# Performance work log

Measured on AMD Instinct MI355X. Metric: run time of the kernel, lower is better.

Reference implementation:

```python
import jax, jax.numpy as jnp
import numpy as np

N = 50000
E = 800000
D_IN, D_HID, D_OUT = 128, 128, 256


def _sage_layer(x, src, dst, W_l, b_l, W_r):
    # PyG SAGEConv: out = lin_l(mean_j x_j) + lin_r(x_i)
    msg = x[src]                                              # [E, d]
    agg = jax.ops.segment_sum(msg, dst, num_segments=x.shape[0])
    cnt = jax.ops.segment_sum(jnp.ones((src.shape[0],), x.dtype), dst,
                              num_segments=x.shape[0])
    mean = agg / jnp.maximum(cnt, 1.0)[:, None]
    return mean @ W_l.T + b_l + x @ W_r.T


def setup_inputs() -> dict:
    key = jax.random.key(0)
    ks = jax.random.split(key, 12)
    x = jax.random.normal(ks[0], (N, D_IN), dtype=jnp.float32)
    edge_index = jax.random.randint(ks[1], (2, E), 0, N, dtype=jnp.int64)

    def lin(k, out_d, in_d):
        s = 1.0 / np.sqrt(in_d)
        return jax.random.uniform(k, (out_d, in_d), jnp.float32, -s, s)

    return {
        "x": x,
        "edge_index": edge_index,
        "W_l0": lin(ks[2], D_HID, D_IN),
        "b_l0": jnp.zeros((D_HID,), jnp.float32),
        "W_r0": lin(ks[3], D_HID, D_IN),
        "W_l1": lin(ks[4], D_HID, D_HID),
        "b_l1": jnp.zeros((D_HID,), jnp.float32),
        "W_r1": lin(ks[5], D_HID, D_HID),
        "W_l2": lin(ks[6], D_OUT, D_HID),
        "b_l2": jnp.zeros((D_OUT,), jnp.float32),
        "W_r2": lin(ks[7], D_OUT, D_HID),
    }


def reference(x, edge_index, W_l0, b_l0, W_r0, W_l1, b_l1, W_r1, W_l2, b_l2, W_r2):
    src, dst = edge_index[0], edge_index[1]
    h = jax.nn.relu(_sage_layer(x, src, dst, W_l0, b_l0, W_r0))   # dropout = identity (eval)
    h = jax.nn.relu(_sage_layer(h, src, dst, W_l1, b_l1, W_r1))
    out = _sage_layer(h, src, dst, W_l2, b_l2, W_r2)
    return out
```

## Files before the change

kernel.cpp:

```cpp
#include <hip/hip_runtime.h>
#include <stdint.h>

typedef unsigned short u16;
typedef unsigned int   u32;
typedef __attribute__((ext_vector_type(8))) short short8;
typedef __attribute__((ext_vector_type(4))) float f32x4;

#define CHUNK 8192

__device__ __forceinline__ u16 f2bf(float f) {
    u32 u = __float_as_uint(f);
    u32 r = (u + 0x7FFFu + ((u >> 16) & 1u)) >> 16;
    return (u16)r;
}

__global__ void detect_fmt(const int* __restrict__ ei, int* __restrict__ flag,
                           int* __restrict__ offs, int N, int E) {
    if (blockIdx.x == 0 && threadIdx.x == 0) {
        int z = ei[1] | ei[3] | ei[5] | ei[7] | ei[9] | ei[11];
        flag[0] = (z == 0) ? 1 : 0;
        offs[N] = E;
    }
}

__global__ void zero_out(float* __restrict__ p, size_t n) {
    size_t i = (size_t)blockIdx.x * 256 + threadIdx.x;
    size_t stride = (size_t)gridDim.x * 256;
    for (; i < n; i += stride) p[i] = 0.f;
}

__global__ void hist_bucket(const int* __restrict__ ei, const int* __restrict__ flag,
                            int* __restrict__ cnt, int E, int N, int nb, int NBK) {
    __shared__ int h[256];
    int b = blockIdx.x, t = threadIdx.x;
    h[t] = 0;
    __syncthreads();
    int is64 = flag[0];
    int base = b * CHUNK;
    int endE = min(base + CHUNK, E);
    for (int i = base + t; i < endE; i += 256) {
        int dst = is64 ? ei[2 * E + 2 * i] : ei[E + i];
        dst = min(max(dst, 0), N - 1);
        atomicAdd(&h[dst >> 8], 1);
    }
    __syncthreads();
    for (int B = t; B < NBK; B += 256) cnt[B * nb + b] = h[B];
}

__global__ void scan_partial(const int* __restrict__ a, int* __restrict__ bsum, int M) {
    __shared__ int sh[256];
    int t = threadIdx.x;
    int idx0 = blockIdx.x * 1024 + t * 4;
    int s = 0;
    #pragma unroll
    for (int i = 0; i < 4; ++i) { int idx = idx0 + i; if (idx < M) s += a[idx]; }
    sh[t] = s;
    __syncthreads();
    #pragma unroll
    for (int off = 128; off > 0; off >>= 1) {
        if (t < off) sh[t] += sh[t + off];
        __syncthreads();
    }
    if (t == 0) bsum[blockIdx.x] = sh[0];
}

__global__ void scan_bsum(int* __restrict__ bsum, int nbs) {
    __shared__ int sh[256];
    __shared__ int carry;
    int t = threadIdx.x;
    if (t == 0) carry = 0;
    __syncthreads();
    for (int base = 0; base < nbs; base += 256) {
        int v = (base + t < nbs) ? bsum[base + t] : 0;
        sh[t] = v;
        __syncthreads();
        #pragma unroll
        for (int off = 1; off < 256; off <<= 1) {
            int x = (t >= off) ? sh[t - off] : 0;
            __syncthreads();
            sh[t] += x;
            __syncthreads();
        }
        if (base + t < nbs) bsum[base + t] = carry + sh[t] - v;
        __syncthreads();
        if (t == 255) carry += sh[255];
        __syncthreads();
    }
}

__global__ void scan_final(int* __restrict__ a, const int* __restrict__ bsum, int M) {
    __shared__ int sh[256];
    int t = threadIdx.x;
    int idx0 = blockIdx.x * 1024 + t * 4;
    int v[4];
    int s = 0;
    #pragma unroll
    for (int i = 0; i < 4; ++i) {
        int idx = idx0 + i;
        v[i] = (idx < M) ? a[idx] : 0;
        s += v[i];
    }
    sh[t] = s;
    __syncthreads();
    #pragma unroll
    for (int off = 1; off < 256; off <<= 1) {
        int x = (t >= off) ? sh[t - off] : 0;
        __syncthreads();
        sh[t] += x;
        __syncthreads();
    }
    int run = sh[t] - s + bsum[blockIdx.x];
    #pragma unroll
    for (int i = 0; i < 4; ++i) {
        int idx = idx0 + i;
        if (idx < M) a[idx] = run;
        run += v[i];
    }
}

__global__ void scatter_pairs(const int* __restrict__ ei, const int* __restrict__ flag,
                              const int* __restrict__ pboff, int2* __restrict__ pairs,
                              int E, int N, int nb, int NBK) {
    __shared__ int cur[256];
    int b = blockIdx.x, t = threadIdx.x;
    for (int B = t; B < NBK; B += 256) cur[B] = pboff[B * nb + b];
    __syncthreads();
    int is64 = flag[0];
    int base = b * CHUNK;
    int endE = min(base + CHUNK, E);
    for (int i = base + t; i < endE; i += 256) {
        int src = is64 ? ei[2 * i] : ei[i];
        int dst = is64 ? ei[2 * E + 2 * i] : ei[E + i];
        src = min(max(src, 0), N - 1);
        dst = min(max(dst, 0), N - 1);
        int slot = atomicAdd(&cur[dst >> 8], 1);
        pairs[slot] = make_int2(src, dst);
    }
}

__global__ void fine_sort(const int2* __restrict__ pairs, const int* __restrict__ pboff,
                          int* __restrict__ offs, int* __restrict__ ssrc,
                          int E, int N, int nb, int NBK) {
    __shared__ int hist[256];
    __shared__ int excl[256];
    __shared__ int cur[256];
    int B = blockIdx.x, t = threadIdx.x;
    int rs = pboff[B * nb];
    int re = (B + 1 < NBK) ? pboff[(B + 1) * nb] : E;
    hist[t] = 0;
    __syncthreads();
    for (int i = rs + t; i < re; i += 256) {
        int2 p = pairs[i];
        atomicAdd(&hist[p.y & 255], 1);
    }
    __syncthreads();
    int v = hist[t];
    excl[t] = v;
    __syncthreads();
    #pragma unroll
    for (int off = 1; off < 256; off <<= 1) {
        int x = (t >= off) ? excl[t - off] : 0;
        __syncthreads();
        excl[t] += x;
        __syncthreads();
    }
    int ex = excl[t] - v;
    int node = B * 256 + t;
    if (node < N) offs[node] = rs + ex;
    cur[t] = rs + ex;
    __syncthreads();
    for (int i = rs + t; i < re; i += 256) {
        int2 p = pairs[i];
        int slot = atomicAdd(&cur[p.y & 255], 1);
        ssrc[slot] = p.x;
    }
}

__global__ void conv_bf16(const float4* __restrict__ x, uint2* __restrict__ H, int n4) {
    int i = blockIdx.x * 256 + threadIdx.x;
    if (i >= n4) return;
    float4 v = x[i];
    uint2 o;
    o.x = ((u32)f2bf(v.y) << 16) | f2bf(v.x);
    o.y = ((u32)f2bf(v.w) << 16) | f2bf(v.z);
    H[i] = o;
}

__global__ void prep_w(const float* __restrict__ Wl, const float* __restrict__ Wr,
                       u16* __restrict__ Wc, int dout) {
    int i = blockIdx.x * 256 + threadIdx.x;
    if (i >= dout * 256) return;
    int j = i >> 8, k = i & 255;
    float v = (k < 128) ? Wl[j * 128 + k] : Wr[j * 128 + (k - 128)];
    Wc[i] = f2bf(v);
}

__device__ __forceinline__ void acc8(float* a, uint4 p) {
    a[0] += __uint_as_float(p.x << 16); a[1] += __uint_as_float(p.x & 0xFFFF0000u);
    a[2] += __uint_as_float(p.y << 16); a[3] += __uint_as_float(p.y & 0xFFFF0000u);
    a[4] += __uint_as_float(p.z << 16); a[5] += __uint_as_float(p.z & 0xFFFF0000u);
    a[6] += __uint_as_float(p.w << 16); a[7] += __uint_as_float(p.w & 0xFFFF0000u);
}

__global__ void aggregate(const u16* __restrict__ H, const int* __restrict__ offs,
                          const int* __restrict__ ssrc, u16* __restrict__ M, int N) {
    int node = blockIdx.x * 16 + (threadIdx.x >> 4);
    int sub  = threadIdx.x & 15;
    if (node >= N) return;
    int beg = offs[node], end = offs[node + 1];
    float a0[8] = {}, a1[8] = {}, a2[8] = {}, a3[8] = {};
    int j = beg;
    for (; j + 3 < end; j += 4) {
        int s0 = ssrc[j], s1 = ssrc[j + 1], s2 = ssrc[j + 2], s3 = ssrc[j + 3];
        uint4 p0 = *(const uint4*)(H + (size_t)s0 * 128 + sub * 8);
        uint4 p1 = *(const uint4*)(H + (size_t)s1 * 128 + sub * 8);
        uint4 p2 = *(const uint4*)(H + (size_t)s2 * 128 + sub * 8);
        uint4 p3 = *(const uint4*)(H + (size_t)s3 * 128 + sub * 8);
        acc8(a0, p0); acc8(a1, p1); acc8(a2, p2); acc8(a3, p3);
    }
    for (; j < end; ++j) {
        uint4 p0 = *(const uint4*)(H + (size_t)ssrc[j] * 128 + sub * 8);
        acc8(a0, p0);
    }
    int d = end - beg;
    float sc = 1.f / (float)(d > 0 ? d : 1);
    #pragma unroll
    for (int i = 0; i < 8; ++i) a0[i] = (a0[i] + a1[i] + a2[i] + a3[i]) * sc;
    uint4 o;
    o.x = ((u32)f2bf(a0[1]) << 16) | f2bf(a0[0]);
    o.y = ((u32)f2bf(a0[3]) << 16) | f2bf(a0[2]);
    o.z = ((u32)f2bf(a0[5]) << 16) | f2bf(a0[4]);
    o.w = ((u32)f2bf(a0[7]) << 16) | f2bf(a0[6]);
    *(uint4*)(M + (size_t)node * 128 + sub * 8) = o;
}

template<int DOUT, bool RELU, bool OUT_F32>
__global__ void gemm_mfma(const u16* __restrict__ M, const u16* __restrict__ H,
                          const u16* __restrict__ Wc, const float* __restrict__ bias,
                          void* __restrict__ out, int N) {
    int tid  = threadIdx.x;
    int w    = tid >> 6;
    int l    = tid & 63;
    int m_base = blockIdx.x * 128 + w * 32;
    int n_base = blockIdx.y * 128;

    int lr = l & 15;
    int lq = l >> 4;
    int kof = lq * 8;

    f32x4 acc[2][8];
    #pragma unroll
    for (int i = 0; i < 2; ++i)
        #pragma unroll
        for (int j = 0; j < 8; ++j) acc[i][j] = (f32x4){0.f, 0.f, 0.f, 0.f};

    int r0 = m_base + lr, r1 = r0 + 16;
    const short8 zf = (short8){0,0,0,0,0,0,0,0};

    #pragma unroll
    for (int ks = 0; ks < 8; ++ks) {
        const u16* Asrc = (ks < 4) ? M : H;
        int ka = (ks & 3) * 32 + kof;
        short8 a0 = (r0 < N) ? *(const short8*)(Asrc + (size_t)r0 * 128 + ka) : zf;
        short8 a1 = (r1 < N) ? *(const short8*)(Asrc + (size_t)r1 * 128 + ka) : zf;
        int kb = ks * 32 + kof;
        #pragma unroll
        for (int ct = 0; ct < 8; ++ct) {
            int wrow = n_base + ct * 16 + lr;
            short8 b = *(const short8*)(Wc + (size_t)wrow * 256 + kb);
            acc[0][ct] = __builtin_amdgcn_mfma_f32_16x16x32_bf16(a0, b, acc[0][ct], 0, 0, 0);
            acc[1][ct] = __builtin_amdgcn_mfma_f32_16x16x32_bf16(a1, b, acc[1][ct], 0, 0, 0);
        }
    }

    #pragma unroll
    for (int rg = 0; rg < 2; ++rg) {
        #pragma unroll
        for (int ct = 0; ct < 8; ++ct) {
            int col = n_base + ct * 16 + lr;
            float bv = bias[col];
            #pragma unroll
            for (int i = 0; i < 4; ++i) {
                int row = m_base + rg * 16 + lq * 4 + i;
                if (row >= N) continue;
                float v = acc[rg][ct][i] + bv;
                if (RELU) v = fmaxf(v, 0.f);
                if (OUT_F32) ((float*)out)[(size_t)row * DOUT + col] = v;
                else         ((u16*)out)[(size_t)row * DOUT + col] = f2bf(v);
            }
        }
    }
}

extern "C" void kernel_launch(void* const* d_in, const int* in_sizes, int n_in,
                              void* d_out, int out_size, void* d_ws, size_t ws_size,
                              hipStream_t stream) {
    const float* x   = (const float*)d_in[0];
    const int*   ei  = (const int*)d_in[1];
    const float* Wl0 = (const float*)d_in[2];
    const float* bl0 = (const float*)d_in[3];
    const float* Wr0 = (const float*)d_in[4];
    const float* Wl1 = (const float*)d_in[5];
    const float* bl1 = (const float*)d_in[6];
    const float* Wr1 = (const float*)d_in[7];
    const float* Wl2 = (const float*)d_in[8];
    const float* bl2 = (const float*)d_in[9];
    const float* Wr2 = (const float*)d_in[10];

    const int N = in_sizes[0] / 128;
    const int E = in_sizes[1] / 2;

    const int NBK = (N + 255) >> 8;
    const int nb  = (E + CHUNK - 1) / CHUNK;
    const int M_  = NBK * nb;
    const int nbs = (M_ + 1023) / 1024;

    size_t off = 0;
    auto alloc = [&](size_t bytes) -> size_t {
        size_t p = off;
        off += (bytes + 255) & ~(size_t)255;
        return p;
    };
    size_t o_flag  = alloc(256);
    size_t o_cnt   = alloc((size_t)M_ * 4);
    size_t o_bsum  = alloc((size_t)nbs * 4);
    size_t o_offs  = alloc(((size_t)N + 1) * 4);
    size_t o_ssrc  = alloc((size_t)E * 4);
    size_t o_pairs = alloc((size_t)E * 8);
    size_t o_Hx    = alloc((size_t)N * 128 * 2);
    size_t o_Ha    = alloc((size_t)N * 128 * 2);
    size_t o_Hb    = alloc((size_t)N * 128 * 2);
    size_t o_Mb    = alloc((size_t)N * 128 * 2);
    size_t o_Wc0   = alloc((size_t)128 * 256 * 2);
    size_t o_Wc1   = alloc((size_t)128 * 256 * 2);
    size_t o_Wc2   = alloc((size_t)256 * 256 * 2);

    if (off > ws_size || NBK > 256) {
        zero_out<<<2048, 256, 0, stream>>>((float*)d_out, (size_t)out_size);
        return;
    }

    char* ws = (char*)d_ws;
    int*  flag  = (int*)(ws + o_flag);
    int*  cnt   = (int*)(ws + o_cnt);
    int*  bsum  = (int*)(ws + o_bsum);
    int*  offs  = (int*)(ws + o_offs);
    int*  ssrc  = (int*)(ws + o_ssrc);
    int2* pairs = (int2*)(ws + o_pairs);
    u16*  Hx    = (u16*)(ws + o_Hx);
    u16*  Ha    = (u16*)(ws + o_Ha);
    u16*  Hb    = (u16*)(ws + o_Hb);
    u16*  Mb    = (u16*)(ws + o_Mb);
    u16*  Wc0   = (u16*)(ws + o_Wc0);
    u16*  Wc1   = (u16*)(ws + o_Wc1);
    u16*  Wc2   = (u16*)(ws + o_Wc2);

    detect_fmt<<<1, 64, 0, stream>>>(ei, flag, offs, N, E);

    hist_bucket<<<nb, 256, 0, stream>>>(ei, flag, cnt, E, N, nb, NBK);
    scan_partial<<<nbs, 256, 0, stream>>>(cnt, bsum, M_);
    scan_bsum<<<1, 256, 0, stream>>>(bsum, nbs);
    scan_final<<<nbs, 256, 0, stream>>>(cnt, bsum, M_);
    scatter_pairs<<<nb, 256, 0, stream>>>(ei, flag, cnt, pairs, E, N, nb, NBK);
    fine_sort<<<NBK, 256, 0, stream>>>(pairs, cnt, offs, ssrc, E, N, nb, NBK);

    int n4 = N * 32;
    conv_bf16<<<(n4 + 255) / 256, 256, 0, stream>>>((const float4*)x, (uint2*)Hx, n4);
    prep_w<<<(128 * 256 + 255) / 256, 256, 0, stream>>>(Wl0, Wr0, Wc0, 128);
    prep_w<<<(128 * 256 + 255) / 256, 256, 0, stream>>>(Wl1, Wr1, Wc1, 128);
    prep_w<<<(256 * 256 + 255) / 256, 256, 0, stream>>>(Wl2, Wr2, Wc2, 256);

    int ab = (N + 15) / 16;
    dim3 g1((N + 127) / 128, 1), g2((N + 127) / 128, 2);

    aggregate<<<ab, 256, 0, stream>>>(Hx, offs, ssrc, Mb, N);
    gemm_mfma<128, true, false><<<g1, 256, 0, stream>>>(Mb, Hx, Wc0, bl0, Ha, N);
    aggregate<<<ab, 256, 0, stream>>>(Ha, offs, ssrc, Mb, N);
    gemm_mfma<128, true, false><<<g1, 256, 0, stream>>>(Mb, Ha, Wc1, bl1, Hb, N);
    aggregate<<<ab, 256, 0, stream>>>(Hb, offs, ssrc, Mb, N);
    gemm_mfma<256, false, true><<<g2, 256, 0, stream>>>(Mb, Hb, Wc2, bl2, d_out, N);
}
```

Baseline: 359.8 us.

## Trim launches, pack sort pairs into u32, halve GEMM row tile

Removes the detect_fmt kernel by having each sorting kernel work out the int64 edge format inline, and merges three weight-prep launches into one. Packs (src, dst&255) into a single 32-bit word, which halves the traffic of the pairs buffer between scatter and fine sort; this adds a guard that N must not exceed 2^17. Shrinks the GEMM tile to 16 rows per wave (64 per block), doubling the grid and reducing per-thread accumulator registers. The smaller tile gives more occupancy and parallelism, but each B fragment is now reused across fewer MFMAs, so weight reads per output rise.

```diff
diff --git a/kernel.cpp b/kernel.cpp
--- a/kernel.cpp
+++ b/kernel.cpp
@@ -14,13 +14,8 @@
     return (u16)r;
 }
 
-__global__ void detect_fmt(const int* __restrict__ ei, int* __restrict__ flag,
-                           int* __restrict__ offs, int N, int E) {
-    if (blockIdx.x == 0 && threadIdx.x == 0) {
-        int z = ei[1] | ei[3] | ei[5] | ei[7] | ei[9] | ei[11];
-        flag[0] = (z == 0) ? 1 : 0;
-        offs[N] = E;
-    }
+__device__ __forceinline__ int edge_is64(const int* __restrict__ ei) {
+    return ((ei[1] | ei[3] | ei[5] | ei[7] | ei[9] | ei[11]) == 0) ? 1 : 0;
 }
 
 __global__ void zero_out(float* __restrict__ p, size_t n) {
@@ -29,13 +24,13 @@
     for (; i < n; i += stride) p[i] = 0.f;
 }
 
-__global__ void hist_bucket(const int* __restrict__ ei, const int* __restrict__ flag,
-                            int* __restrict__ cnt, int E, int N, int nb, int NBK) {
+__global__ void hist_bucket(const int* __restrict__ ei, int* __restrict__ cnt,
+                            int E, int N, int nb, int NBK) {
     __shared__ int h[256];
     int b = blockIdx.x, t = threadIdx.x;
     h[t] = 0;
     __syncthreads();
-    int is64 = flag[0];
+    int is64 = edge_is64(ei);
     int base = b * CHUNK;
     int endE = min(base + CHUNK, E);
     for (int i = base + t; i < endE; i += 256) {
@@ -118,14 +113,13 @@
     }
 }
 
-__global__ void scatter_pairs(const int* __restrict__ ei, const int* __restrict__ flag,
-                              const int* __restrict__ pboff, int2* __restrict__ pairs,
-                              int E, int N, int nb, int NBK) {
+__global__ void scatter_pairs(const int* __restrict__ ei, const int* __restrict__ pboff,
+                              u32* __restrict__ pairs, int E, int N, int nb, int NBK) {
     __shared__ int cur[256];
     int b = blockIdx.x, t = threadIdx.x;
     for (int B = t; B < NBK; B += 256) cur[B] = pboff[B * nb + b];
     __syncthreads();
-    int is64 = flag[0];
+    int is64 = edge_is64(ei);
     int base = b * CHUNK;
     int endE = min(base + CHUNK, E);
     for (int i = base + t; i < endE; i += 256) {
@@ -134,24 +128,25 @@
         src = min(max(src, 0), N - 1);
         dst = min(max(dst, 0), N - 1);
         int slot = atomicAdd(&cur[dst >> 8], 1);
-        pairs[slot] = make_int2(src, dst);
-    }
-}
-
-__global__ void fine_sort(const int2* __restrict__ pairs, const int* __restrict__ pboff,
+        pairs[slot] = (u32)src | ((u32)(dst & 255) << 17);
+    }
+}
+
+__global__ void fine_sort(const u32* __restrict__ pairs, const int* __restrict__ pboff,
                           int* __restrict__ offs, int* __restrict__ ssrc,
                           int E, int N, int nb, int NBK) {
     __shared__ int hist[256];
     __shared__ int excl[256];
     __shared__ int cur[256];
     int B = blockIdx.x, t = threadIdx.x;
+    if (B == 0 && t == 0) offs[N] = E;
     int rs = pboff[B * nb];
     int re = (B + 1 < NBK) ? pboff[(B + 1) * nb] : E;
     hist[t] = 0;
     __syncthreads();
     for (int i = rs + t; i < re; i += 256) {
-        int2 p = pairs[i];
-        atomicAdd(&hist[p.y & 255], 1);
+        u32 p = pairs[i];
+        atomicAdd(&hist[(p >> 17) & 255], 1);
     }
     __syncthreads();
     int v = hist[t];
@@ -170,9 +165,9 @@
     cur[t] = rs + ex;
     __syncthreads();
     for (int i = rs + t; i < re; i += 256) {
-        int2 p = pairs[i];
-        int slot = atomicAdd(&cur[p.y & 255], 1);
-        ssrc[slot] = p.x;
+        u32 p = pairs[i];
+        int slot = atomicAdd(&cur[(p >> 17) & 255], 1);
+        ssrc[slot] = (int)(p & 0x1FFFFu);
     }
 }
 
@@ -186,13 +181,19 @@
     H[i] = o;
 }
 
-__global__ void prep_w(const float* __restrict__ Wl, const float* __restrict__ Wr,
-                       u16* __restrict__ Wc, int dout) {
+__global__ void prep_w_all(const float* __restrict__ Wl0, const float* __restrict__ Wr0,
+                           const float* __restrict__ Wl1, const float* __restrict__ Wr1,
+                           const float* __restrict__ Wl2, const float* __restrict__ Wr2,
+                           u16* __restrict__ Wc0, u16* __restrict__ Wc1,
+                           u16* __restrict__ Wc2) {
     int i = blockIdx.x * 256 + threadIdx.x;
-    if (i >= dout * 256) return;
-    int j = i >> 8, k = i & 255;
+    const float* Wl; const float* Wr; u16* Wc; int base;
+    if (i < 32768)      { Wl = Wl0; Wr = Wr0; Wc = Wc0; base = i; }
+    else if (i < 65536) { Wl = Wl1; Wr = Wr1; Wc = Wc1; base = i - 32768; }
+    else                { Wl = Wl2; Wr = Wr2; Wc = Wc2; base = i - 65536; }
+    int j = base >> 8, k = base & 255;
     float v = (k < 128) ? Wl[j * 128 + k] : Wr[j * 128 + (k - 128)];
-    Wc[i] = f2bf(v);
+    Wc[base] = f2bf(v);
 }
 
 __device__ __forceinline__ void acc8(float* a, uint4 p) {
@@ -241,20 +242,18 @@
     int tid  = threadIdx.x;
     int w    = tid >> 6;
     int l    = tid & 63;
-    int m_base = blockIdx.x * 128 + w * 32;
+    int m_base = blockIdx.x * 64 + w * 16;
     int n_base = blockIdx.y * 128;
 
     int lr = l & 15;
     int lq = l >> 4;
     int kof = lq * 8;
 
-    f32x4 acc[2][8];
-    #pragma unroll
-    for (int i = 0; i < 2; ++i)
-        #pragma unroll
-        for (int j = 0; j < 8; ++j) acc[i][j] = (f32x4){0.f, 0.f, 0.f, 0.f};
-
-    int r0 = m_base + lr, r1 = r0 + 16;
+    f32x4 acc[8];
+    #pragma unroll
+    for (int j = 0; j < 8; ++j) acc[j] = (f32x4){0.f, 0.f, 0.f, 0.f};
+
+    int r0 = m_base + lr;
     const short8 zf = (short8){0,0,0,0,0,0,0,0};
 
     #pragma unroll
@@ -262,32 +261,27 @@
         const u16* Asrc = (ks < 4) ? M : H;
         int ka = (ks & 3) * 32 + kof;
         short8 a0 = (r0 < N) ? *(const short8*)(Asrc + (size_t)r0 * 128 + ka) : zf;
-        short8 a1 = (r1 < N) ? *(const short8*)(Asrc + (size_t)r1 * 128 + ka) : zf;
         int kb = ks * 32 + kof;
         #pragma unroll
         for (int ct = 0; ct < 8; ++ct) {
             int wrow = n_base + ct * 16 + lr;
             short8 b = *(const short8*)(Wc + (size_t)wrow * 256 + kb);
-            acc[0][ct] = __builtin_amdgcn_mfma_f32_16x16x32_bf16(a0, b, acc[0][ct], 0, 0, 0);
-            acc[1][ct] = __builtin_amdgcn_mfma_f32_16x16x32_bf16(a1, b, acc[1][ct], 0, 0, 0);
+            acc[ct] = __builtin_amdgcn_mfma_f32_16x16x32_bf16(a0, b, acc[ct], 0, 0, 0);
         }
     }
 
     #pragma unroll
-    for (int rg = 0; rg < 2; ++rg) {
+    for (int ct = 0; ct < 8; ++ct) {
+        int col = n_base + ct * 16 + lr;
+        float bv = bias[col];
         #pragma unroll
-        for (int ct = 0; ct < 8; ++ct) {
-            int col = n_base + ct * 16 + lr;
-            float bv = bias[col];
-            #pragma unroll
-            for (int i = 0; i < 4; ++i) {
-                int row = m_base + rg * 16 + lq * 4 + i;
-                if (row >= N) continue;
-                float v = acc[rg][ct][i] + bv;
-                if (RELU) v = fmaxf(v, 0.f);
-                if (OUT_F32) ((float*)out)[(size_t)row * DOUT + col] = v;
-                else         ((u16*)out)[(size_t)row * DOUT + col] = f2bf(v);
-            }
+        for (int i = 0; i < 4; ++i) {
+            int row = m_base + lq * 4 + i;
+            if (row >= N) continue;
+            float v = acc[ct][i] + bv;
+            if (RELU) v = fmaxf(v, 0.f);
+            if (OUT_F32) ((float*)out)[(size_t)row * DOUT + col] = v;
+            else         ((u16*)out)[(size_t)row * DOUT + col] = f2bf(v);
         }
     }
 }
@@ -321,12 +315,11 @@
         off += (bytes + 255) & ~(size_t)255;
         return p;
     };
-    size_t o_flag  = alloc(256);
     size_t o_cnt   = alloc((size_t)M_ * 4);
     size_t o_bsum  = alloc((size_t)nbs * 4);
     size_t o_offs  = alloc(((size_t)N + 1) * 4);
     size_t o_ssrc  = alloc((size_t)E * 4);
-    size_t o_pairs = alloc((size_t)E * 8);
+    size_t o_pairs = alloc((size_t)E * 4);
     size_t o_Hx    = alloc((size_t)N * 128 * 2);
     size_t o_Ha    = alloc((size_t)N * 128 * 2);
     size_t o_Hb    = alloc((size_t)N * 128 * 2);
@@ -335,18 +328,17 @@
     size_t o_Wc1   = alloc((size_t)128 * 256 * 2);
     size_t o_Wc2   = alloc((size_t)256 * 256 * 2);
 
-    if (off > ws_size || NBK > 256) {
+    if (off > ws_size || NBK > 256 || N > (1 << 17)) {
         zero_out<<<2048, 256, 0, stream>>>((float*)d_out, (size_t)out_size);
         return;
     }
 
     char* ws = (char*)d_ws;
-    int*  flag  = (int*)(ws + o_flag);
     int*  cnt   = (int*)(ws + o_cnt);
     int*  bsum  = (int*)(ws + o_bsum);
     int*  offs  = (int*)(ws + o_offs);
     int*  ssrc  = (int*)(ws + o_ssrc);
-    int2* pairs = (int2*)(ws + o_pairs);
+    u32*  pairs = (u32*)(ws + o_pairs);
     u16*  Hx    = (u16*)(ws + o_Hx);
     u16*  Ha    = (u16*)(ws + o_Ha);
     u16*  Hb    = (u16*)(ws + o_Hb);
@@ -355,23 +347,19 @@
     u16*  Wc1   = (u16*)(ws + o_Wc1);
     u16*  Wc2   = (u16*)(ws + o_Wc2);
 
-    detect_fmt<<<1, 64, 0, stream>>>(ei, flag, offs, N, E);
-
-    hist_bucket<<<nb, 256, 0, stream>>>(ei, flag, cnt, E, N, nb, NBK);
+    hist_bucket<<<nb, 256, 0, stream>>>(ei, cnt, E, N, nb, NBK);
     scan_partial<<<nbs, 256, 0, stream>>>(cnt, bsum, M_);
     scan_bsum<<<1, 256, 0, stream>>>(bsum, nbs);
     scan_final<<<nbs, 256, 0, stream>>>(cnt, bsum, M_);
-    scatter_pairs<<<nb, 256, 0, stream>>>(ei, flag, cnt, pairs, E, N, nb, NBK);
+    scatter_pairs<<<nb, 256, 0, stream>>>(ei, cnt, pairs, E, N, nb, NBK);
     fine_sort<<<NBK, 256, 0, stream>>>(pairs, cnt, offs, ssrc, E, N, nb, NBK);
 
     int n4 = N * 32;
     conv_bf16<<<(n4 + 255) / 256, 256, 0, stream>>>((const float4*)x, (uint2*)Hx, n4);
-    prep_w<<<(128 * 256 + 255) / 256, 256, 0, stream>>>(Wl0, Wr0, Wc0, 128);
-    prep_w<<<(128 * 256 + 255) / 256, 256, 0, stream>>>(Wl1, Wr1, Wc1, 128);
-    prep_w<<<(256 * 256 + 255) / 256, 256, 0, stream>>>(Wl2, Wr2, Wc2, 256);
+    prep_w_all<<<512, 256, 0, stream>>>(Wl0, Wr0, Wl1, Wr1, Wl2, Wr2, Wc0, Wc1, Wc2);
 
     int ab = (N + 15) / 16;
-    dim3 g1((N + 127) / 128, 1), g2((N + 127) / 128, 2);
+    dim3 g1((N + 63) / 64, 1), g2((N + 63) / 64, 2);
 
     aggregate<<<ab, 256, 0, stream>>>(Hx, offs, ssrc, Mb, N);
     gemm_mfma<128, true, false><<<g1, 256, 0, stream>>>(Mb, Hx, Wc0, bl0, Ha, N);
```

Measured after the change: 400.5 us. +11.3%, slower.
